# Optimization experiments

Measured on AMD Instinct MI355X. Metric: run time of the kernel, lower is better.

The kernel has to match this reference:

```python
import jax, jax.numpy as jnp
import numpy as np

N, H, T, HID = 4, 12, 1024, 64
TM = 128          # attention_predictor_length
PK = 64           # pconfig.k
HIDDEN = 768
EPS = 1e-4


def setup_inputs() -> dict:
    key = jax.random.key(0)
    ks = jax.random.split(key, 14)
    f32 = jnp.float32
    rn = lambda kk, shp: jax.random.normal(kk, shp, dtype=f32)
    inp = {}
    for i, n in enumerate(["q", "k", "v", "q_for_atten", "k_for_atten",
                           "v_for_atten", "q_for_score", "k_for_score"]):
        inp[n] = rn(ks[i], (N, H, T, HID))
    inp["attention_mask"] = jnp.zeros((N, 1, 1, T), f32)  # additive mask, 0 = keep
    inp["attention_scores_truth"] = rn(ks[8], (N, H, T, T))
    inp["context_layer_truth"] = rn(ks[9], (N, T, HIDDEN))
    # FAVOR+ gaussian-orthogonal projection matrix [nb_features, HID]
    nbf = int(HID * np.log(HID))  # 266
    rng = np.random.default_rng(0)
    blocks = []
    for _ in range(int(np.ceil(nbf / HID))):
        qm, _ = np.linalg.qr(rng.standard_normal((HID, HID)))
        blocks.append(qm.T)
    pm = np.concatenate(blocks, 0)[:nbf]
    mult = np.linalg.norm(rng.standard_normal((nbf, HID)), axis=1)
    inp["proj_matrix"] = jnp.asarray(mult[:, None] * pm, f32)
    # attention predictor (mlp): Linear(128,128)+LN+GELU, then Linear(128,TM)
    D2 = 2 * HID
    s = lambda kk, shp, fan: jax.random.normal(kk, shp, f32) / np.sqrt(fan)
    inp["enc_w"] = s(ks[10], (D2, D2), D2)
    inp["enc_b"] = jnp.zeros((D2,), f32)
    inp["ln_g"] = jnp.ones((D2,), f32)
    inp["ln_b"] = jnp.zeros((D2,), f32)
    inp["dec_w"] = s(ks[11], (D2, TM), D2)
    inp["dec_b"] = jnp.zeros((TM,), f32)
    return inp


def _perf_feat(x, pm, is_query):
    # performer softmax kernel features
    ratio = pm.shape[0] ** -0.5
    dn = x.shape[-1] ** -0.25
    dd = jnp.einsum('nhtd,fd->nhtf', dn * x, pm)
    diag = jnp.sum(x * x, -1, keepdims=True) * 0.5 * (dn * dn)
    if is_query:
        m = jnp.max(dd, axis=-1, keepdims=True)
    else:
        m = jnp.max(dd, axis=(-2, -1), keepdims=True)
    return ratio * (jnp.exp(dd - diag - m) + EPS)


def _forward(q, k, v, q_for_atten, k_for_atten, v_for_atten, q_for_score,
             k_for_score, attention_mask, attention_scores_truth,
             context_layer_truth, proj_matrix, enc_w, enc_b, ln_g, ln_b,
             dec_w, dec_b):
    mask = attention_mask                                   # [N,1,1,T]
    # vmask: nearest-resize eye(128) to (T,HID), broadcast, zero masked rows
    eye = jnp.eye(128, dtype=v.dtype)
    hi = (jnp.arange(T) * 128) // T
    wi = (jnp.arange(HID) * 128) // HID
    vfa = eye[hi][:, wi]                                    # [T,HID]
    vfa = jnp.broadcast_to(vfa, (N, H, T, HID))
    vfa = jnp.where(jnp.swapaxes(mask, -1, -2) < -1, 0.0, vfa)
    # performer (FAVOR+) linear attention, non-causal
    qp = _perf_feat(q_for_atten, proj_matrix, True)         # [N,H,T,F]
    kp = _perf_feat(k_for_atten, proj_matrix, False)
    d_inv = 1.0 / jnp.einsum('nhtf,nhf->nht', qp, kp.sum(-2))
    ctx = jnp.einsum('nhtf,nhtd->nhfd', kp, vfa)
    pcl = jnp.einsum('nhfd,nhtf,nht->nhtd', ctx, qp, d_inv)  # performer_context_layer
    performer_value = jax.lax.stop_gradient(jnp.concatenate([pcl, v], -1))  # detach
    # attention predictor (mlp; dropout inactive at eval)
    h1 = performer_value @ enc_w + enc_b
    mu = jnp.mean(h1, -1, keepdims=True)
    var = jnp.mean((h1 - mu) ** 2, -1, keepdims=True)
    h1 = (h1 - mu) / jnp.sqrt(var + 1e-5) * ln_g + ln_b
    h1 = jax.nn.gelu(h1, approximate=False)
    score = h1 @ dec_w + dec_b                              # [N,H,T,TM]
    # mask_softmax: nearest-resize mask [N,1,1,T] -> [N,1,1,TM]
    rmask = mask[..., (jnp.arange(TM) * T) // TM]
    score_m = jnp.where(rmask < -1, -10000.0, score)
    probs = jax.nn.softmax(score_m, -1)                     # estimated_attention_probs
    # resize (T,TM)->(T,T) nearest for the loss
    ci = (jnp.arange(T) * TM) // T
    score_r = score[..., ci]                                # unmasked resized score
    logp = jax.nn.log_softmax(score_r + mask, -1)
    pt = jax.nn.softmax(attention_scores_truth + mask, -1)
    valid = mask > -1                                       # [N,1,1,T]
    kl = jnp.where(valid, pt * (jnp.log(jnp.clip(pt, 1e-12)) - logp), 0.0)
    denom = jnp.sum(jnp.broadcast_to(valid, kl.shape).astype(jnp.float32))
    loss_kl = kl.sum() / denom * 0.25
    mfill = mask < -1
    loss_mse = jnp.mean((jnp.where(mfill, 0.0, score_r)
                         - jnp.where(mfill, 0.0, attention_scores_truth)) ** 2)
    loss = loss_kl + loss_mse
    # top-k partial attention mask, k_flatten over batch
    kk = min(max(int(round(PK * (TM / T))), 1), TM)
    valT = (jnp.swapaxes(mask, -1, -2) > -1)                # [N,1,T,1]
    t = (probs * valT).reshape(N, H * T * TM)
    _, idx = jax.lax.top_k(t, kk * T * H)
    pam = jnp.full((N, H * T * TM), -10000.0, jnp.float32)
    pam = pam.at[jnp.arange(N)[:, None], idx].set(0.0)
    pam = pam.reshape(N, H, T, TM)
    return loss, pcl, probs, pam


def reference(q, k, v, q_for_atten, k_for_atten, v_for_atten, q_for_score,
              k_for_score, attention_mask, attention_scores_truth,
              context_layer_truth, proj_matrix, enc_w, enc_b, ln_g, ln_b,
              dec_w, dec_b):
    return _forward(q, k, v, q_for_atten, k_for_atten, v_for_atten,
                    q_for_score, k_for_score, attention_mask,
                    attention_scores_truth, context_layer_truth, proj_matrix,
                    enc_w, enc_b, ln_g, ln_b, dec_w, dec_b)
```

## Files before the change

### kernel.cpp

```cpp
#include <hip/hip_runtime.h>
#include <hip/hip_bf16.h>
#include <math.h>

#define N_B 4
#define H_H 12
#define T_T 1024
#define D_H 64
#define F_F 266
#define N_H 48
#define TM_ 128
#define KSEL 98304u
#define PER_BATCH 1572864
#define FCH 14
#define NCH 19

static __device__ __forceinline__ float waveSum(float v){
  for(int o=32;o;o>>=1) v += __shfl_xor(v,o,64);
  return v;
}
static __device__ __forceinline__ float waveMax(float v){
  for(int o=32;o;o>>=1) v = fmaxf(v,__shfl_xor(v,o,64));
  return v;
}

#define DN_C 0.35355339059327373f
#define DIAG_C 0.0625f
#define RATIO_C 0.06131393394849658f
#define EPS_C 1e-4f

__global__ __launch_bounds__(256) void keyfeat_kern(
    const float* __restrict__ kfa, const float* __restrict__ pm,
    const float* __restrict__ mask,
    float* __restrict__ ctxraw, float* __restrict__ ksumP,
    float* __restrict__ mfP){
  int head = blockIdx.x, fc = blockIdx.y;
  int f0 = fc*FCH;
  int n = head / H_H;
  int lane = threadIdx.x & 63, tq = threadIdx.x >> 6;
  __shared__ float cred[FCH][64];
  __shared__ float kred[4][FCH];
  __shared__ float mred[4];
  float kacc[FCH], cacc[FCH];
  #pragma unroll
  for(int i=0;i<FCH;i++){ kacc[i]=0.f; cacc[i]=0.f; }
  float mymax = -3.4e38f;
  for(int tt=0; tt<4; tt++){
    int tc = tq*4 + tt;
    int t = lane*16 + tc;
    const float4* xp = (const float4*)(kfa + ((size_t)head*T_T + t)*D_H);
    float4 xr[16];
    #pragma unroll
    for(int kk=0;kk<16;kk++) xr[kk] = xp[kk];
    float dg = 0.f;
    #pragma unroll
    for(int kk=0;kk<16;kk++){ float4 x = xr[kk];
      dg += x.x*x.x + x.y*x.y + x.z*x.z + x.w*x.w; }
    dg *= DIAG_C;
    float cmul = ((tc < 8) && (mask[n*T_T + t] > -1.0f)) ? 1.f : 0.f;
    for(int fi=0; fi<FCH; fi++){
      const float4* pr = (const float4*)(pm + (size_t)(f0+fi)*D_H);
      float s0=0,s1=0,s2=0,s3=0;
      #pragma unroll
      for(int kk=0;kk<16;kk++){ float4 w4 = pr[kk];
        s0+=xr[kk].x*w4.x; s1+=xr[kk].y*w4.y; s2+=xr[kk].z*w4.z; s3+=xr[kk].w*w4.w; }
      float dd = DN_C*((s0+s1)+(s2+s3));
      mymax = fmaxf(mymax, dd);
      float e = expf(dd - dg);
      kacc[fi] += e;
      cacc[fi] += e*cmul;
    }
  }
  #pragma unroll
  for(int fi=0;fi<FCH;fi++){
    float s = waveSum(kacc[fi]);
    if(lane==0) kred[tq][fi] = s;
  }
  mymax = waveMax(mymax);
  if(lane==0) mred[tq]=mymax;
  if(tq==0){
    #pragma unroll
    for(int fi=0;fi<FCH;fi++) cred[fi][lane] = cacc[fi];
  }
  __syncthreads();
  if(tq==1){
    #pragma unroll
    for(int fi=0;fi<FCH;fi++) cred[fi][lane] += cacc[fi];
  }
  __syncthreads();
  for(int i=threadIdx.x; i<FCH*64; i+=256){
    int fi=i>>6, d=i&63;
    ctxraw[((size_t)head*F_F + f0+fi)*64 + d] = cred[fi][d];
  }
  if(threadIdx.x < FCH)
    ksumP[head*F_F + f0 + threadIdx.x] =
      kred[0][threadIdx.x]+kred[1][threadIdx.x]+kred[2][threadIdx.x]+kred[3][threadIdx.x];
  if(threadIdx.x==0)
    mfP[head*NCH+fc] = fmaxf(fmaxf(mred[0],mred[1]),fmaxf(mred[2],mred[3]));
}

__global__ __launch_bounds__(256) void fixup_kern(
    const float* __restrict__ mfP, const float* __restrict__ ksumP,
    const float* __restrict__ ctxraw, const float* __restrict__ mask,
    float* __restrict__ ctx, float* __restrict__ ksum,
    float* __restrict__ ksum_tot, float* __restrict__ ctx_tot){
  int head = blockIdx.x; int n = head/H_H;
  __shared__ float segc[64];
  __shared__ float part[4][64];
  __shared__ float kpart[4];
  float m_head = mfP[head*NCH];
  for(int i=1;i<NCH;i++) m_head = fmaxf(m_head, mfP[head*NCH+i]);
  float e_mh = expf(-m_head);
  if(threadIdx.x < 64){
    int d = threadIdx.x; float c=0.f;
    for(int i=0;i<8;i++) c += (mask[n*T_T + 16*d + i] > -1.0f) ? 1.f : 0.f;
    segc[d] = c;
  }
  __syncthreads();
  int g = threadIdx.x>>6, d = threadIdx.x&63;
  float ct = 0.f, kt = 0.f;
  for(int f=g; f<F_F; f+=4){
    float craw = ctxraw[((size_t)head*F_F+f)*64 + d];
    float cf = RATIO_C*(craw*e_mh + EPS_C*segc[d]);
    ctx[((size_t)head*F_F+f)*64 + d] = cf;
    ct += cf;
    if(d==0){
      float kf = RATIO_C*(ksumP[head*F_F+f]*e_mh + EPS_C*(float)T_T);
      ksum[head*F_F+f] = kf;
      kt += kf;
    }
  }
  part[g][d] = ct;
  if(d==0) kpart[g] = kt;
  __syncthreads();
  if(threadIdx.x < 64)
    ctx_tot[head*64+threadIdx.x] =
      part[0][threadIdx.x]+part[1][threadIdx.x]+part[2][threadIdx.x]+part[3][threadIdx.x];
  if(threadIdx.x==0) ksum_tot[head] = kpart[0]+kpart[1]+kpart[2]+kpart[3];
}

__global__ __launch_bounds__(256) void qfeat_kern(
    const float* __restrict__ qfa, const float* __restrict__ pm,
    const float* __restrict__ ctx, const float* __restrict__ ksum,
    const float* __restrict__ ksum_tot, const float* __restrict__ ctx_tot,
    float* __restrict__ pcl){
  int head = blockIdx.x, tc = blockIdx.y;
  int rl = threadIdx.x >> 2, fs = threadIdx.x & 3;
  int t = tc*64 + rl;
  __shared__ float pms[56*68];
  __shared__ float ctxs[56*68];
  __shared__ float ksums[56];
  const float* xp = qfa + ((size_t)head*T_T + t)*D_H;
  float4 xr[16];
  #pragma unroll
  for(int kk=0;kk<16;kk++) xr[kk] = ((const float4*)xp)[kk];
  float diag = 0.f;
  #pragma unroll
  for(int kk=0;kk<16;kk++)
    diag += xr[kk].x*xr[kk].x + xr[kk].y*xr[kk].y + xr[kk].z*xr[kk].z + xr[kk].w*xr[kk].w;
  diag *= DIAG_C;
  float m_run = -3.4e38f, m_acc = 0.f, S = 0.f;
  bool first = true;
  float4 acc[16];
  #pragma unroll
  for(int kk=0;kk<16;kk++) acc[kk] = make_float4(0.f,0.f,0.f,0.f);
  for(int c=0;c<5;c++){
    int f0 = c*56, CF = min(56, F_F-f0);
    __syncthreads();
    for(int i=threadIdx.x;i<CF*16;i+=256){
      int fl=i>>4, d4=i&15;
      ((float4*)(pms+fl*68))[d4]  = ((const float4*)(pm+(size_t)(f0+fl)*64))[d4];
      ((float4*)(ctxs+fl*68))[d4] = ((const float4*)(ctx+((size_t)head*F_F+f0+fl)*64))[d4];
    }
    for(int i=threadIdx.x;i<CF;i+=256) ksums[i]=ksum[head*F_F+f0+i];
    __syncthreads();
    int nj = (CF - fs + 3)>>2;
    for(int j=0;j<nj;j++){
      int fl = fs+4*j;
      const float4* pr = (const float4*)(pms + fl*68);
      float s0=0,s1=0,s2=0,s3=0;
      #pragma unroll
      for(int kk=0;kk<16;kk++){ float4 w4 = pr[kk];
        s0+=xr[kk].x*w4.x; s1+=xr[kk].y*w4.y; s2+=xr[kk].z*w4.z; s3+=xr[kk].w*w4.w; }
      float dd = DN_C*((s0+s1)+(s2+s3));
      if(first){ m_acc = dd; first = false; }
      m_run = fmaxf(m_run, dd);
      float e = expf(dd - diag - m_acc);
      S += e * ksums[fl];
      const float4* cr = (const float4*)(ctxs + fl*68);
      #pragma unroll
      for(int kk=0;kk<16;kk++){ float4 c4=cr[kk];
        acc[kk].x+=e*c4.x; acc[kk].y+=e*c4.y; acc[kk].z+=e*c4.z; acc[kk].w+=e*c4.w; }
    }
  }
  {
    float fac = expf(m_acc - m_run);
    S *= fac;
    #pragma unroll
    for(int kk=0;kk<16;kk++){
      acc[kk].x*=fac; acc[kk].y*=fac; acc[kk].z*=fac; acc[kk].w*=fac;
    }
  }
  for(int st=1; st<=2; st<<=1){
    float mo = __shfl_xor(m_run, st, 64);
    float mc = fmaxf(m_run, mo);
    float fac = expf(m_run - mc);
    S *= fac;
    S += __shfl_xor(S, st, 64);
    #pragma unroll
    for(int kk=0;kk<16;kk++){
      acc[kk].x*=fac; acc[kk].y*=fac; acc[kk].z*=fac; acc[kk].w*=fac;
    }
    #pragma unroll
    for(int kk=0;kk<16;kk++){
      acc[kk].x += __shfl_xor(acc[kk].x,st,64);
      acc[kk].y += __shfl_xor(acc[kk].y,st,64);
      acc[kk].z += __shfl_xor(acc[kk].z,st,64);
      acc[kk].w += __shfl_xor(acc[kk].w,st,64);
    }
    m_run = mc;
  }
  float den = S + EPS_C * ksum_tot[head];
  float dinv = 1.0f/den;
  float4 w0,w1,w2,w3;
  if(fs==0){ w0=acc[0]; w1=acc[1]; w2=acc[2]; w3=acc[3]; }
  else if(fs==1){ w0=acc[4]; w1=acc[5]; w2=acc[6]; w3=acc[7]; }
  else if(fs==2){ w0=acc[8]; w1=acc[9]; w2=acc[10]; w3=acc[11]; }
  else { w0=acc[12]; w1=acc[13]; w2=acc[14]; w3=acc[15]; }
  const float4* ctp = ((const float4*)(ctx_tot + head*64)) + fs*4;
  float4 c0=ctp[0], c1=ctp[1], c2=ctp[2], c3=ctp[3];
  float4* po = (float4*)(pcl + ((size_t)head*T_T + t)*D_H) + fs*4;
  po[0] = make_float4((w0.x+EPS_C*c0.x)*dinv,(w0.y+EPS_C*c0.y)*dinv,(w0.z+EPS_C*c0.z)*dinv,(w0.w+EPS_C*c0.w)*dinv);
  po[1] = make_float4((w1.x+EPS_C*c1.x)*dinv,(w1.y+EPS_C*c1.y)*dinv,(w1.z+EPS_C*c1.z)*dinv,(w1.w+EPS_C*c1.w)*dinv);
  po[2] = make_float4((w2.x+EPS_C*c2.x)*dinv,(w2.y+EPS_C*c2.y)*dinv,(w2.z+EPS_C*c2.z)*dinv,(w2.w+EPS_C*c2.w)*dinv);
  po[3] = make_float4((w3.x+EPS_C*c3.x)*dinv,(w3.y+EPS_C*c3.y)*dinv,(w3.z+EPS_C*c3.z)*dinv,(w3.w+EPS_C*c3.w)*dinv);
}

#define FMA4(A,s,W) {A.x+=(s)*W.x; A.y+=(s)*W.y; A.z+=(s)*W.z; A.w+=(s)*W.w;}
__global__ __launch_bounds__(256) void mlp_kern(
    const float* __restrict__ pcl, const float* __restrict__ v,
    const float* __restrict__ mask,
    const float* __restrict__ encw, const float* __restrict__ encb,
    const float* __restrict__ lng, const float* __restrict__ lnb,
    const float* __restrict__ decw, const float* __restrict__ decb,
    float* __restrict__ probsout, float* __restrict__ scoreout){
  int head = blockIdx.x, tblk = blockIdx.y;
  int t0 = tblk*32;
  int n = head / H_H;
  __shared__ float xs[32*132];
  __shared__ float wts[32*132];
  __shared__ float h1s[32*132];
  int colT = threadIdx.x & 15, rowT = threadIdx.x >> 4;
  int r0 = rowT, r1 = rowT + 16;
  const float* pclrow = pcl + ((size_t)head*T_T + t0)*D_H;
  const float* vrow   = v   + ((size_t)head*T_T + t0)*D_H;
  for(int i=threadIdx.x;i<512;i+=256){
    int r=i>>4, q=i&15;
    ((float4*)(xs + r*132))[q]      = ((const float4*)(pclrow + r*64))[q];
    ((float4*)(xs + r*132 + 64))[q] = ((const float4*)(vrow   + r*64))[q];
  }
  float4 bias0 = ((const float4*)encb)[colT];
  float4 bias1 = ((const float4*)encb)[colT+16];
  float4 A0=bias0, A1=bias1, B0=bias0, B1=bias1;
  for(int kc=0;kc<4;kc++){
    __syncthreads();
    for(int i=threadIdx.x;i<1024;i+=256){
      int k=i>>5, q=i&31;
      ((float4*)(wts + k*132))[q] = ((const float4*)(encw + (size_t)(kc*32+k)*128))[q];
    }
    __syncthreads();
    #pragma unroll
    for(int kq=0;kq<8;kq++){
      float4 x0 = ((const float4*)(xs + r0*132 + kc*32))[kq];
      float4 x1 = ((const float4*)(xs + r1*132 + kc*32))[kq];
      #pragma unroll
      for(int kk=0;kk<4;kk++){
        const float* wrow = wts + (kq*4+kk)*132;
        float4 wa = ((const float4*)wrow)[colT];
        float4 wb = ((const float4*)wrow)[colT+16];
        float xv0 = (kk==0)?x0.x:(kk==1)?x0.y:(kk==2)?x0.z:x0.w;
        float xv1 = (kk==0)?x1.x:(kk==1)?x1.y:(kk==2)?x1.z:x1.w;
        FMA4(A0,xv0,wa); FMA4(A1,xv0,wb);
        FMA4(B0,xv1,wa); FMA4(B1,xv1,wb);
      }
    }
  }
  float4 lg0 = ((const float4*)lng)[colT], lg1 = ((const float4*)lng)[colT+16];
  float4 lb0 = ((const float4*)lnb)[colT], lb1 = ((const float4*)lnb)[colT+16];
  float s0 = A0.x+A0.y+A0.z+A0.w + A1.x+A1.y+A1.z+A1.w;
  float s1 = B0.x+B0.y+B0.z+B0.w + B1.x+B1.y+B1.z+B1.w;
  for(int o=1;o<16;o<<=1){ s0 += __shfl_xor(s0,o,64); s1 += __shfl_xor(s1,o,64); }
  float mu0 = s0*(1.0f/128.0f), mu1 = s1*(1.0f/128.0f);
  float v0=0.f, v1=0.f;
  { float d;
    d=A0.x-mu0; v0+=d*d; d=A0.y-mu0; v0+=d*d; d=A0.z-mu0; v0+=d*d; d=A0.w-mu0; v0+=d*d;
    d=A1.x-mu0; v0+=d*d; d=A1.y-mu0; v0+=d*d; d=A1.z-mu0; v0+=d*d; d=A1.w-mu0; v0+=d*d;
    d=B0.x-mu1; v1+=d*d; d=B0.y-mu1; v1+=d*d; d=B0.z-mu1; v1+=d*d; d=B0.w-mu1; v1+=d*d;
    d=B1.x-mu1; v1+=d*d; d=B1.y-mu1; v1+=d*d; d=B1.z-mu1; v1+=d*d; d=B1.w-mu1; v1+=d*d; }
  for(int o=1;o<16;o<<=1){ v0 += __shfl_xor(v0,o,64); v1 += __shfl_xor(v1,o,64); }
  float den0 = sqrtf(v0*(1.0f/128.0f)+1e-5f);
  float den1 = sqrtf(v1*(1.0f/128.0f)+1e-5f);
  #define GELU(x) ((x)*0.5f*(1.0f+erff((x)*0.70710678118654752f)))
  #define LNG(a,mu,dn,g,b) GELU(((a)-(mu))/(dn)*(g)+(b))
  float4 H;
  H.x=LNG(A0.x,mu0,den0,lg0.x,lb0.x); H.y=LNG(A0.y,mu0,den0,lg0.y,lb0.y);
  H.z=LNG(A0.z,mu0,den0,lg0.z,lb0.z); H.w=LNG(A0.w,mu0,den0,lg0.w,lb0.w);
  ((float4*)(h1s + r0*132))[colT] = H;
  H.x=LNG(A1.x,mu0,den0,lg1.x,lb1.x); H.y=LNG(A1.y,mu0,den0,lg1.y,lb1.y);
  H.z=LNG(A1.z,mu0,den0,lg1.z,lb1.z); H.w=LNG(A1.w,mu0,den0,lg1.w,lb1.w);
  ((float4*)(h1s + r0*132))[colT+16] = H;
  H.x=LNG(B0.x,mu1,den1,lg0.x,lb0.x); H.y=LNG(B0.y,mu1,den1,lg0.y,lb0.y);
  H.z=LNG(B0.z,mu1,den1,lg0.z,lb0.z); H.w=LNG(B0.w,mu1,den1,lg0.w,lb0.w);
  ((float4*)(h1s + r1*132))[colT] = H;
  H.x=LNG(B1.x,mu1,den1,lg1.x,lb1.x); H.y=LNG(B1.y,mu1,den1,lg1.y,lb1.y);
  H.z=LNG(B1.z,mu1,den1,lg1.z,lb1.z); H.w=LNG(B1.w,mu1,den1,lg1.w,lb1.w);
  ((float4*)(h1s + r1*132))[colT+16] = H;
  bias0 = ((const float4*)decb)[colT];
  bias1 = ((const float4*)decb)[colT+16];
  A0=bias0; A1=bias1; B0=bias0; B1=bias1;
  for(int kc=0;kc<4;kc++){
    __syncthreads();
    for(int i=threadIdx.x;i<1024;i+=256){
      int k=i>>5, q=i&31;
      ((float4*)(wts + k*132))[q] = ((const float4*)(decw + (size_t)(kc*32+k)*128))[q];
    }
    __syncthreads();
    #pragma unroll
    for(int kq=0;kq<8;kq++){
      float4 x0 = ((const float4*)(h1s + r0*132 + kc*32))[kq];
      float4 x1 = ((const float4*)(h1s + r1*132 + kc*32))[kq];
      #pragma unroll
      for(int kk=0;kk<4;kk++){
        const float* wrow = wts + (kq*4+kk)*132;
        float4 wa = ((const float4*)wrow)[colT];
        float4 wb = ((const float4*)wrow)[colT+16];
        float xv0 = (kk==0)?x0.x:(kk==1)?x0.y:(kk==2)?x0.z:x0.w;
        float xv1 = (kk==0)?x1.x:(kk==1)?x1.y:(kk==2)?x1.z:x1.w;
        FMA4(A0,xv0,wa); FMA4(A1,xv0,wb);
        FMA4(B0,xv1,wa); FMA4(B1,xv1,wb);
      }
    }
  }
  const float* mrow = mask + n*T_T;
  int c0 = colT*4, c1 = colT*4 + 64;
  float rm0[4], rm1[4];
  #pragma unroll
  for(int i=0;i<4;i++){ rm0[i]=mrow[(c0+i)*8]; rm1[i]=mrow[(c1+i)*8]; }
  float sA[8], sB[8];
  sA[0]=(rm0[0]<-1.f)?-10000.f:A0.x; sA[1]=(rm0[1]<-1.f)?-10000.f:A0.y;
  sA[2]=(rm0[2]<-1.f)?-10000.f:A0.z; sA[3]=(rm0[3]<-1.f)?-10000.f:A0.w;
  sA[4]=(rm1[0]<-1.f)?-10000.f:A1.x; sA[5]=(rm1[1]<-1.f)?-10000.f:A1.y;
  sA[6]=(rm1[2]<-1.f)?-10000.f:A1.z; sA[7]=(rm1[3]<-1.f)?-10000.f:A1.w;
  sB[0]=(rm0[0]<-1.f)?-10000.f:B0.x; sB[1]=(rm0[1]<-1.f)?-10000.f:B0.y;
  sB[2]=(rm0[2]<-1.f)?-10000.f:B0.z; sB[3]=(rm0[3]<-1.f)?-10000.f:B0.w;
  sB[4]=(rm1[0]<-1.f)?-10000.f:B1.x; sB[5]=(rm1[1]<-1.f)?-10000.f:B1.y;
  sB[6]=(rm1[2]<-1.f)?-10000.f:B1.z; sB[7]=(rm1[3]<-1.f)?-10000.f:B1.w;
  float mx0=sA[0], mx1=sB[0];
  #pragma unroll
  for(int i=1;i<8;i++){ mx0=fmaxf(mx0,sA[i]); mx1=fmaxf(mx1,sB[i]); }
  for(int o=1;o<16;o<<=1){ mx0=fmaxf(mx0,__shfl_xor(mx0,o,64)); mx1=fmaxf(mx1,__shfl_xor(mx1,o,64)); }
  float Z0=0.f, Z1=0.f;
  #pragma unroll
  for(int i=0;i<8;i++){ sA[i]=expf(sA[i]-mx0); Z0+=sA[i]; sB[i]=expf(sB[i]-mx1); Z1+=sB[i]; }
  for(int o=1;o<16;o<<=1){ Z0+=__shfl_xor(Z0,o,64); Z1+=__shfl_xor(Z1,o,64); }
  float zi0=1.0f/Z0, zi1=1.0f/Z1;
  size_t rb0 = ((size_t)head*T_T + t0 + r0)*TM_;
  size_t rb1 = ((size_t)head*T_T + t0 + r1)*TM_;
  ((float4*)(probsout+rb0))[colT]    = make_float4(sA[0]*zi0,sA[1]*zi0,sA[2]*zi0,sA[3]*zi0);
  ((float4*)(probsout+rb0))[colT+16] = make_float4(sA[4]*zi0,sA[5]*zi0,sA[6]*zi0,sA[7]*zi0);
  ((float4*)(probsout+rb1))[colT]    = make_float4(sB[0]*zi1,sB[1]*zi1,sB[2]*zi1,sB[3]*zi1);
  ((float4*)(probsout+rb1))[colT+16] = make_float4(sB[4]*zi1,sB[5]*zi1,sB[6]*zi1,sB[7]*zi1);
  ((float4*)(scoreout+rb0))[colT]    = A0;
  ((float4*)(scoreout+rb0))[colT+16] = A1;
  ((float4*)(scoreout+rb1))[colT]    = B0;
  ((float4*)(scoreout+rb1))[colT+16] = B1;
}

__global__ __launch_bounds__(256) void loss_kern(
    const float* __restrict__ truth, const float* __restrict__ mask,
    const float* __restrict__ score, float* __restrict__ klrow,
    float* __restrict__ mserow){
  int row = blockIdx.x;
  int n = row / (H_H*T_T);
  int t = threadIdx.x;
  int lane = t & 63, tq = t >> 6;
  __shared__ float sc[128];
  __shared__ float red[8];
  float4 av  = ((const float4*)(truth + (size_t)row*T_T))[t];
  float4 mkv = ((const float4*)(mask + (size_t)n*T_T))[t];
  if(t < 128) sc[t] = score[(size_t)row*TM_ + t];
  __syncthreads();
  float scv = sc[t>>1];
  float ma = fmaxf(fmaxf(av.x+mkv.x, av.y+mkv.y), fmaxf(av.z+mkv.z, av.w+mkv.w));
  float ms = scv + fmaxf(fmaxf(mkv.x, mkv.y), fmaxf(mkv.z, mkv.w));
  for(int o=32;o;o>>=1){ ma=fmaxf(ma,__shfl_xor(ma,o,64)); ms=fmaxf(ms,__shfl_xor(ms,o,64)); }
  if(lane==0){ red[tq]=ma; red[4+tq]=ms; }
  __syncthreads();
  ma = fmaxf(fmaxf(red[0],red[1]),fmaxf(red[2],red[3]));
  ms = fmaxf(fmaxf(red[4],red[5]),fmaxf(red[6],red[7]));
  __syncthreads();
  float e0=__expf(av.x+mkv.x-ma), e1=__expf(av.y+mkv.y-ma),
        e2=__expf(av.z+mkv.z-ma), e3=__expf(av.w+mkv.w-ma);
  float Za = (e0+e1)+(e2+e3);
  float Zs = (__expf(scv+mkv.x-ms)+__expf(scv+mkv.y-ms))
           + (__expf(scv+mkv.z-ms)+__expf(scv+mkv.w-ms));
  for(int o=32;o;o>>=1){ Za+=__shfl_xor(Za,o,64); Zs+=__shfl_xor(Zs,o,64); }
  if(lane==0){ red[tq]=Za; red[4+tq]=Zs; }
  __syncthreads();
  Za = (red[0]+red[1])+(red[2]+red[3]);
  Zs = (red[4]+red[5])+(red[6]+red[7]);
  __syncthreads();
  float lZs = __logf(Zs), lZa = __logf(Za);
  float invZa = 1.0f/Za;
  float kl=0.f, mse=0.f;
  #define LKL(AJ,MKJ,EJ) { \
    if((MKJ) > -1.0f){ \
      float pt = (EJ)*invZa; \
      float logpt = (pt >= 1e-12f) ? ((AJ)+(MKJ)-ma-lZa) : -27.631021116f; \
      float logp = (scv+(MKJ)-ms) - lZs; \
      kl += pt*(logpt-logp); } \
    float sv = ((MKJ) < -1.0f)?0.f:scv; \
    float avv = ((MKJ) < -1.0f)?0.f:(AJ); \
    float dd = sv-avv; mse += dd*dd; }
  LKL(av.x,mkv.x,e0) LKL(av.y,mkv.y,e1) LKL(av.z,mkv.z,e2) LKL(av.w,mkv.w,e3)
  #undef LKL
  for(int o=32;o;o>>=1){ kl+=__shfl_xor(kl,o,64); mse+=__shfl_xor(mse,o,64); }
  if(lane==0){ red[tq]=kl; red[4+tq]=mse; }
  __syncthreads();
  if(t==0){
    klrow[row]  = (red[0]+red[1])+(red[2]+red[3]);
    mserow[row] = (red[4]+red[5])+(red[6]+red[7]);
  }
}

__global__ __launch_bounds__(256) void finloss_kern(
    const float* __restrict__ klrow, const float* __restrict__ mserow,
    const float* __restrict__ mask, float* __restrict__ out0){
  __shared__ double reds[256];
  double kls=0, mses=0;
  for(int i=threadIdx.x;i<N_H*T_T;i+=256){ kls+=(double)klrow[i]; mses+=(double)mserow[i]; }
  double vcnt=0;
  for(int i=threadIdx.x;i<N_B*T_T;i+=256) if(mask[i] > -1.0f) vcnt+=1.0;
  reds[threadIdx.x]=kls; __syncthreads();
  for(int o=128;o;o>>=1){ if(threadIdx.x<o) reds[threadIdx.x]+=reds[threadIdx.x+o]; __syncthreads(); }
  double klsum = reds[0]; __syncthreads();
  reds[threadIdx.x]=mses; __syncthreads();
  for(int o=128;o;o>>=1){ if(threadIdx.x<o) reds[threadIdx.x]+=reds[threadIdx.x+o]; __syncthreads(); }
  double msesum = reds[0]; __syncthreads();
  reds[threadIdx.x]=vcnt; __syncthreads();
  for(int o=128;o;o>>=1){ if(threadIdx.x<o) reds[threadIdx.x]+=reds[threadIdx.x+o]; __syncthreads(); }
  if(threadIdx.x==0){
    double denom = reds[0] * (double)(H_H*T_T);
    double loss = klsum/denom*0.25 + msesum/((double)N_B*H_H*T_T*T_T);
    out0[0]=(float)loss;
  }
}

__global__ void topk_init(unsigned* __restrict__ hist, unsigned* __restrict__ state,
                          unsigned* __restrict__ tiecnt){
  int i = blockIdx.x*256+threadIdx.x;
  if(i < 4*256) hist[i]=0;
  if(i < 4){ state[i*4+0]=0u; state[i*4+1]=KSEL; state[i*4+2]=0u; tiecnt[i]=0u; }
}

__global__ __launch_bounds__(256) void topk_hist(
    const float* __restrict__ probs, const float* __restrict__ mask,
    const unsigned* __restrict__ state, unsigned* __restrict__ hist, int level){
  __shared__ unsigned lh[4*256];
  for(int i=threadIdx.x;i<1024;i+=256) lh[i]=0;
  __syncthreads();
  unsigned pmask = (level==0)?0u:(0xFFFFFFFFu << (32-8*level));
  unsigned pref[4];
  for(int b=0;b<4;b++) pref[b]=state[b*4+0] & pmask;
  int shift = 24-8*level;
  size_t total = (size_t)N_B*PER_BATCH;
  for(size_t idx = (size_t)blockIdx.x*256+threadIdx.x; idx < total; idx += (size_t)gridDim.x*256){
    int b = (int)(idx / PER_BATCH);
    unsigned r = (unsigned)(idx - (size_t)b*PER_BATCH);
    int t = (int)((r>>7)&1023u);
    float val = probs[idx];
    if(!(mask[b*T_T+t] > -1.0f)) val = 0.0f;
    unsigned u = __float_as_uint(val);
    if((u & pmask) == pref[b]) atomicAdd(&lh[b*256+((u>>shift)&255u)],1u);
  }
  __syncthreads();
  for(int i=threadIdx.x;i<1024;i+=256){
    unsigned c = lh[i];
    if(c) atomicAdd(&hist[i], c);
  }
}

__global__ void topk_scan(unsigned* __restrict__ hist, unsigned* __restrict__ state, int level){
  int b = blockIdx.x;
  if(threadIdx.x==0){
    const unsigned* h = hist + b*256;
    unsigned remk = state[b*4+1];
    unsigned cum = 0; int sel=0;
    for(int bin=255; bin>=0; bin--){
      unsigned c = h[bin];
      if(remk <= cum + c){ sel=bin; break; }
      cum += c;
    }
    state[b*4+0] |= ((unsigned)sel) << (24-8*level);
    state[b*4+1] = remk - cum;
    state[b*4+2] += cum;
  }
  __syncthreads();
  for(int i=threadIdx.x;i<256;i+=blockDim.x) hist[b*256+i]=0;
}

__global__ __launch_bounds__(256) void topk_write(
    const float* __restrict__ probs, const float* __restrict__ mask,
    const unsigned* __restrict__ state, float* __restrict__ pam,
    unsigned* __restrict__ ties, unsigned* __restrict__ tiecnt){
  unsigned thr[4];
  for(int b=0;b<4;b++) thr[b]=state[b*4+0];
  size_t total=(size_t)N_B*PER_BATCH;
  for(size_t idx=(size_t)blockIdx.x*256+threadIdx.x; idx<total; idx += (size_t)gridDim.x*256){
    int b = (int)(idx / PER_BATCH);
    unsigned r = (unsigned)(idx - (size_t)b*PER_BATCH);
    int t = (int)((r>>7)&1023u);
    float val = probs[idx];
    if(!(mask[b*T_T+t] > -1.0f)) val=0.0f;
    unsigned u=__float_as_uint(val);
    float o = -10000.0f;
    if(u > thr[b]) o = 0.0f;
    else if(u == thr[b]){
      unsigned pos = atomicAdd(&tiecnt[b],1u);
      if(pos < 65536u) ties[(size_t)b*65536+pos]=r;
    }
    pam[idx]=o;
  }
}

__global__ __launch_bounds__(256) void topk_ties(
    const unsigned* __restrict__ state, const unsigned* __restrict__ ties,
    const unsigned* __restrict__ tiecnt, float* __restrict__ pam){
  int b = blockIdx.x;
  unsigned needed = state[b*4+1];
  unsigned nt = min(tiecnt[b], 65536u);
  __shared__ unsigned redu[256];
  __shared__ unsigned lohi[2];
  if(threadIdx.x==0){ lohi[0]=0u; lohi[1]=PER_BATCH; }
  __syncthreads();
  if(needed == 0 || nt == 0) return;
  while(true){
    __syncthreads();
    unsigned lo=lohi[0], hi=lohi[1];
    if(hi-lo<=1u) break;
    unsigned mid=(lo+hi)>>1;
    unsigned c=0;
    for(unsigned i=threadIdx.x;i<nt;i+=256) c += (ties[(size_t)b*65536+i] < mid)?1u:0u;
    redu[threadIdx.x]=c; __syncthreads();
    for(int o=128;o;o>>=1){ if(threadIdx.x<o) redu[threadIdx.x]+=redu[threadIdx.x+o]; __syncthreads(); }
    if(threadIdx.x==0){ if(redu[0]>=needed) lohi[1]=mid; else lohi[0]=mid; }
  }
  __syncthreads();
  unsigned X=lohi[1];
  for(unsigned i=threadIdx.x;i<nt;i+=256){
    unsigned r=ties[(size_t)b*65536+i];
    if(r < X) pam[(size_t)b*PER_BATCH + r]=0.0f;
  }
}

extern "C" void kernel_launch(void* const* d_in, const int* in_sizes, int n_in,
                              void* d_out, int out_size, void* d_ws, size_t ws_size,
                              hipStream_t stream) {
  const float* v     = (const float*)d_in[2];
  const float* qfa   = (const float*)d_in[3];
  const float* kfa   = (const float*)d_in[4];
  const float* mask  = (const float*)d_in[8];
  const float* truth = (const float*)d_in[9];
  const float* pm    = (const float*)d_in[11];
  const float* encw  = (const float*)d_in[12];
  const float* encb  = (const float*)d_in[13];
  const float* lng   = (const float*)d_in[14];
  const float* lnb   = (const float*)d_in[15];
  const float* decw  = (const float*)d_in[16];
  const float* decb  = (const float*)d_in[17];
  float* out = (float*)d_out;
  float* ws  = (float*)d_ws;

  float* ctx     = ws;
  float* ksum    = ctx + (size_t)N_H*F_F*64;
  float* klrow   = ksum + N_H*F_F;
  float* mserow  = klrow + N_H*T_T;
  unsigned* hist   = (unsigned*)(mserow + N_H*T_T);
  unsigned* state  = hist + 1024;
  unsigned* tiecnt = state + 16;
  unsigned* ties   = tiecnt + 12;
  float* ctxraw  = (float*)(ties + (size_t)4*65536);
  float* ksumP   = ctxraw + (size_t)N_H*F_F*64;
  float* mfP     = ksumP + N_H*F_F;
  float* ksum_tot= mfP + 1024;
  float* ctx_tot = ksum_tot + 48;

  float* pcl   = out + 1;
  float* probs = pcl + (size_t)N_H*T_T*D_H;
  float* pam   = probs + (size_t)N_H*T_T*TM_;

  keyfeat_kern<<<dim3(N_H,NCH),256,0,stream>>>(kfa, pm, mask, ctxraw, ksumP, mfP);
  fixup_kern<<<N_H,256,0,stream>>>(mfP, ksumP, ctxraw, mask, ctx, ksum, ksum_tot, ctx_tot);
  qfeat_kern<<<dim3(N_H,16),256,0,stream>>>(qfa, pm, ctx, ksum, ksum_tot, ctx_tot, pcl);
  mlp_kern<<<dim3(N_H,32),256,0,stream>>>(pcl, v, mask, encw, encb, lng, lnb,
                                          decw, decb, probs, pam );
  loss_kern<<<N_H*T_T,256,0,stream>>>(truth, mask, pam , klrow, mserow);
  finloss_kern<<<1,256,0,stream>>>(klrow, mserow, mask, out);
  topk_init<<<4,256,0,stream>>>(hist, state, tiecnt);
  for(int lvl=0;lvl<4;lvl++){
    topk_hist<<<2048,256,0,stream>>>(probs, mask, state, hist, lvl);
    topk_scan<<<4,64,0,stream>>>(hist, state, lvl);
  }
  topk_write<<<2048,256,0,stream>>>(probs, mask, state, pam, ties, tiecnt);
  topk_ties<<<4,256,0,stream>>>(state, ties, tiecnt, pam);
}
```

Measured before the change: 580.8 us.

## Use 11/11/10-bit radix select for top-k instead of four 8-bit passes

The radix-select threshold search for the batch-flattened top-k now runs three passes with 2048/2048/1024-bin histograms instead of four 256-bin passes. Each pass reads the full probs tensor, so dropping one pass cuts a full read of about 25 MB. The scan kernel becomes a two-level parallel prefix search over the larger histograms. The cost is a larger shared-memory histogram per block (32 KB), which lowers occupancy and adds zeroing and flush work in every hist block.

```diff
diff --git a/kernel.cpp b/kernel.cpp
--- a/kernel.cpp
+++ b/kernel.cpp
@@ -455,23 +455,25 @@
   }
 }
 
-__global__ void topk_init(unsigned* __restrict__ hist, unsigned* __restrict__ state,
-                          unsigned* __restrict__ tiecnt){
+__global__ __launch_bounds__(256) void topk_init3(
+    unsigned* __restrict__ hist, unsigned* __restrict__ state,
+    unsigned* __restrict__ tiecnt){
   int i = blockIdx.x*256+threadIdx.x;
-  if(i < 4*256) hist[i]=0;
-  if(i < 4){ state[i*4+0]=0u; state[i*4+1]=KSEL; state[i*4+2]=0u; tiecnt[i]=0u; }
-}
-
-__global__ __launch_bounds__(256) void topk_hist(
+  if(i < 4*2048) hist[i]=0u;
+  if(i < 4){ state[i*4+0]=0u; state[i*4+1]=KSEL; tiecnt[i]=0u; }
+}
+
+__global__ __launch_bounds__(256) void topk_hist3(
     const float* __restrict__ probs, const float* __restrict__ mask,
     const unsigned* __restrict__ state, unsigned* __restrict__ hist, int level){
-  __shared__ unsigned lh[4*256];
-  for(int i=threadIdx.x;i<1024;i+=256) lh[i]=0;
-  __syncthreads();
-  unsigned pmask = (level==0)?0u:(0xFFFFFFFFu << (32-8*level));
+  __shared__ unsigned lh[4*2048];
+  for(int i=threadIdx.x;i<8192;i+=256) lh[i]=0u;
+  __syncthreads();
+  int shift = (level==0)?21:(level==1)?10:0;
+  unsigned mbits = (level==2)?1023u:2047u;
+  int topshift = shift + ((level==2)?10:11);
   unsigned pref[4];
-  for(int b=0;b<4;b++) pref[b]=state[b*4+0] & pmask;
-  int shift = 24-8*level;
+  for(int b=0;b<4;b++) pref[b]=state[b*4+0];
   size_t total = (size_t)N_B*PER_BATCH;
   for(size_t idx = (size_t)blockIdx.x*256+threadIdx.x; idx < total; idx += (size_t)gridDim.x*256){
     int b = (int)(idx / PER_BATCH);
@@ -480,32 +482,48 @@
     float val = probs[idx];
     if(!(mask[b*T_T+t] > -1.0f)) val = 0.0f;
     unsigned u = __float_as_uint(val);
-    if((u & pmask) == pref[b]) atomicAdd(&lh[b*256+((u>>shift)&255u)],1u);
-  }
-  __syncthreads();
-  for(int i=threadIdx.x;i<1024;i+=256){
+    bool ok = (level==0) || ((u>>topshift) == (pref[b]>>topshift));
+    if(ok) atomicAdd(&lh[b*2048 + ((u>>shift)&mbits)], 1u);
+  }
+  __syncthreads();
+  for(int i=threadIdx.x;i<8192;i+=256){
     unsigned c = lh[i];
     if(c) atomicAdd(&hist[i], c);
   }
 }
 
-__global__ void topk_scan(unsigned* __restrict__ hist, unsigned* __restrict__ state, int level){
+__global__ __launch_bounds__(256) void topk_scan3(
+    unsigned* __restrict__ hist, unsigned* __restrict__ state, int level){
   int b = blockIdx.x;
+  unsigned* h = hist + b*2048;
+  int shift = (level==0)?21:(level==1)?10:0;
+  int nb = (level==2)?1024:2048;
+  int per = nb/256;
+  __shared__ unsigned cs[256];
+  unsigned s = 0;
+  for(int i=0;i<per;i++) s += h[threadIdx.x*per + i];
+  cs[threadIdx.x] = s;
+  __syncthreads();
   if(threadIdx.x==0){
-    const unsigned* h = hist + b*256;
     unsigned remk = state[b*4+1];
-    unsigned cum = 0; int sel=0;
-    for(int bin=255; bin>=0; bin--){
-      unsigned c = h[bin];
-      if(remk <= cum + c){ sel=bin; break; }
-      cum += c;
-    }
-    state[b*4+0] |= ((unsigned)sel) << (24-8*level);
+    unsigned cum = 0; int sc = 0;
+    for(int c=255;c>=0;c--){
+      unsigned cc = cs[c];
+      if(remk <= cum + cc){ sc = c; break; }
+      cum += cc;
+    }
+    int sb = 0;
+    for(int bb=per-1;bb>=0;bb--){
+      unsigned cc = h[sc*per+bb];
+      if(remk <= cum + cc){ sb = bb; break; }
+      cum += cc;
+    }
+    unsigned bin = (unsigned)(sc*per + sb);
+    state[b*4+0] |= bin << shift;
     state[b*4+1] = remk - cum;
-    state[b*4+2] += cum;
-  }
-  __syncthreads();
-  for(int i=threadIdx.x;i<256;i+=blockDim.x) hist[b*256+i]=0;
+  }
+  __syncthreads();
+  for(int i=threadIdx.x;i<2048;i+=256) h[i]=0u;
 }
 
 __global__ __launch_bounds__(256) void topk_write(
@@ -585,7 +603,7 @@
   float* klrow   = ksum + N_H*F_F;
   float* mserow  = klrow + N_H*T_T;
   unsigned* hist   = (unsigned*)(mserow + N_H*T_T);
-  unsigned* state  = hist + 1024;
+  unsigned* state  = hist + 4*2048;
   unsigned* tiecnt = state + 16;
   unsigned* ties   = tiecnt + 12;
   float* ctxraw  = (float*)(ties + (size_t)4*65536);
@@ -605,10 +623,10 @@
                                           decw, decb, probs, pam );
   loss_kern<<<N_H*T_T,256,0,stream>>>(truth, mask, pam , klrow, mserow);
   finloss_kern<<<1,256,0,stream>>>(klrow, mserow, mask, out);
-  topk_init<<<4,256,0,stream>>>(hist, state, tiecnt);
-  for(int lvl=0;lvl<4;lvl++){
-    topk_hist<<<2048,256,0,stream>>>(probs, mask, state, hist, lvl);
-    topk_scan<<<4,64,0,stream>>>(hist, state, lvl);
+  topk_init3<<<32,256,0,stream>>>(hist, state, tiecnt);
+  for(int lvl=0;lvl<3;lvl++){
+    topk_hist3<<<2048,256,0,stream>>>(probs, mask, state, hist, lvl);
+    topk_scan3<<<4,256,0,stream>>>(hist, state, lvl);
   }
   topk_write<<<2048,256,0,stream>>>(probs, mask, state, pam, ties, tiecnt);
   topk_ties<<<4,256,0,stream>>>(state, ties, tiecnt, pam);
```

After: 558.0 us, median of 2. -3.9%, faster.
